# Optimization experiments

Measured on AMD Instinct MI355X. Metric: run time of the kernel, lower is better.

The kernel has to match this reference:

```python
import jax, jax.numpy as jnp
import numpy as np

TOP_K = 2  # config.top_k


def setup_inputs() -> dict:
    key = jax.random.key(0)
    k0, k1, k2, k3, k4 = jax.random.split(key, 5)
    B, S, D, F, E = 1, 2048, 512, 1024, 8
    scale = 0.02
    hidden_states = jax.random.normal(k0, (B, S, D), dtype=jnp.float32)
    router_w = jax.random.normal(k1, (D, E), dtype=jnp.float32) * scale
    w1 = jax.random.normal(k2, (E, D, F), dtype=jnp.float32) * scale  # gate proj
    w2 = jax.random.normal(k3, (E, F, D), dtype=jnp.float32) * scale  # down proj
    w3 = jax.random.normal(k4, (E, D, F), dtype=jnp.float32) * scale  # up proj
    return {"hidden_states": hidden_states, "router_w": router_w,
            "w1": w1, "w2": w2, "w3": w3}


def reference(hidden_states, router_w, w1, w2, w3):
    B, S, D = hidden_states.shape
    E = router_w.shape[1]
    x = hidden_states.reshape(-1, D)                      # [T, D]
    T = x.shape[0]

    # router: softmax in float32, top-k, renormalize (matches torch source)
    router_logits = x @ router_w                          # [T, E]
    probs = jax.nn.softmax(router_logits.astype(jnp.float32), axis=-1)
    routing_weights, selected_experts = jax.lax.top_k(probs, TOP_K)  # [T, K]
    routing_weights = routing_weights / routing_weights.sum(axis=-1, keepdims=True)
    routing_weights = routing_weights.astype(x.dtype)

    # combine weights: scatter top-k weights into dense [T, E] (one-hot combine)
    combine = jnp.zeros((T, E), dtype=x.dtype).at[
        jnp.arange(T)[:, None], selected_experts].add(routing_weights)

    # dense-all-experts evaluation, math-identical to gather-GEMM-scatter:
    # unselected experts get combine weight 0 and contribute nothing.
    gate = jax.nn.silu(jnp.einsum('td,edf->tef', x, w1))  # [T, E, F]
    up = jnp.einsum('td,edf->tef', x, w3)                 # [T, E, F]
    h = gate * up * combine[:, :, None]                   # weight before down-proj
    out = jnp.einsum('tef,efd->td', h, w2)                # [T, D]
    return out.reshape(B, S, D)
```

## Files before the change

kernel.cpp:

```cpp
#include <hip/hip_runtime.h>
#include <hip/hip_bf16.h>


typedef __attribute__((ext_vector_type(4))) float f32x4;
typedef __attribute__((ext_vector_type(8))) __bf16 bf16x8;

#define T_TOK 2048
#define DMODEL 512
#define FFN 1024
#define NE 8
#define MAXMB 40
#define PCAP (MAXMB * 128)

__device__ __forceinline__ void gload_lds16(const void* g, void* l) {
  __builtin_amdgcn_global_load_lds(
      (const __attribute__((address_space(1))) void*)g,
      (__attribute__((address_space(3))) void*)l, 16, 0, 0);
}

#define PIPE_BAR_8()                                        \
  asm volatile("s_waitcnt vmcnt(8)" ::: "memory");          \
  __builtin_amdgcn_s_barrier();                             \
  __builtin_amdgcn_sched_barrier(0)
#define PIPE_BAR_6()                                        \
  asm volatile("s_waitcnt vmcnt(6)" ::: "memory");          \
  __builtin_amdgcn_s_barrier();                             \
  __builtin_amdgcn_sched_barrier(0)
#define PIPE_BAR_0()                                        \
  asm volatile("s_waitcnt vmcnt(0)" ::: "memory");          \
  __builtin_amdgcn_s_barrier();                             \
  __builtin_amdgcn_sched_barrier(0)
#define POST_BAR()                                          \
  __builtin_amdgcn_s_barrier();                             \
  __builtin_amdgcn_sched_barrier(0)

__global__ __launch_bounds__(256) void prep_kernel(
    const float* __restrict__ x, const float* __restrict__ rw,
    const float* __restrict__ w1, const float* __restrict__ w2,
    const float* __restrict__ w3, __bf16* __restrict__ xb,
    __bf16* __restrict__ w1t, __bf16* __restrict__ w2t,
    __bf16* __restrict__ w3t, int* __restrict__ tope, float* __restrict__ topw,
    int* __restrict__ pair_t, float* __restrict__ pair_w,
    int* __restrict__ sched_e) {
  __shared__ __bf16 tile[64][65];
  const int bx = blockIdx.x;
  const int tid = threadIdx.x;

  if (bx < 3072) {
    const float* src;
    __bf16* dst;
    int R, C, idx;
    if (bx < 1024)      { src = w1; dst = w1t; R = 512;  C = 1024; idx = bx; }
    else if (bx < 2048) { src = w3; dst = w3t; R = 512;  C = 1024; idx = bx - 1024; }
    else                { src = w2; dst = w2t; R = 1024; C = 512;  idx = bx - 2048; }
    const int ntx = C >> 6, nty = R >> 6;
    const int cx = idx % ntx;
    const int gry = idx / ntx;
    const int e = gry / nty;
    const int r0 = (gry % nty) * 64;
    const int c0 = cx * 64;
    src += (size_t)e * R * C;
    dst += (size_t)e * R * C;
#pragma unroll
    for (int q = 0; q < 4; ++q) {
      const int r = (tid >> 4) + q * 16;
      const int c = (tid & 15) * 4;
      const f32x4 v = *(const f32x4*)&src[(size_t)(r0 + r) * C + c0 + c];
      tile[r][c] = (__bf16)v[0];
      tile[r][c + 1] = (__bf16)v[1];
      tile[r][c + 2] = (__bf16)v[2];
      tile[r][c + 3] = (__bf16)v[3];
    }
    __syncthreads();
#pragma unroll
    for (int p = 0; p < 2; ++p) {
      const int cc = (tid >> 3) + p * 32;
      const int rr = (tid & 7) * 8;
      union { bf16x8 v; __bf16 s[8]; } u;
#pragma unroll
      for (int i = 0; i < 8; ++i) u.s[i] = tile[rr + i][cc];
      *(bf16x8*)&dst[(size_t)(c0 + cc) * R + r0 + rr] = u.v;
    }
  } else if (bx < 3584) {
    const int t = (bx - 3072) * 4 + (tid >> 6);
    const int lane = tid & 63;
    const float* xr = x + (size_t)t * DMODEL + lane * 8;
    const f32x4 a = *(const f32x4*)xr;
    const f32x4 b = *(const f32x4*)(xr + 4);
    bf16x8 v;
    v[0] = (__bf16)a[0]; v[1] = (__bf16)a[1]; v[2] = (__bf16)a[2]; v[3] = (__bf16)a[3];
    v[4] = (__bf16)b[0]; v[5] = (__bf16)b[1]; v[6] = (__bf16)b[2]; v[7] = (__bf16)b[3];
    *(bf16x8*)&xb[(size_t)t * DMODEL + lane * 8] = v;

    float xv[8] = {a[0], a[1], a[2], a[3], b[0], b[1], b[2], b[3]};
    float part[NE];
#pragma unroll
    for (int e = 0; e < NE; ++e) part[e] = 0.f;
#pragma unroll
    for (int i = 0; i < 8; ++i) {
      const int d = lane * 8 + i;
      const f32x4 r0 = *(const f32x4*)&rw[(size_t)d * NE];
      const f32x4 r1 = *(const f32x4*)&rw[(size_t)d * NE + 4];
      part[0] += xv[i] * r0[0]; part[1] += xv[i] * r0[1];
      part[2] += xv[i] * r0[2]; part[3] += xv[i] * r0[3];
      part[4] += xv[i] * r1[0]; part[5] += xv[i] * r1[1];
      part[6] += xv[i] * r1[2]; part[7] += xv[i] * r1[3];
    }
#pragma unroll
    for (int off = 32; off > 0; off >>= 1) {
#pragma unroll
      for (int e = 0; e < NE; ++e) part[e] += __shfl_xor(part[e], off);
    }
    if (lane == 0) {
      int ia = 0;
#pragma unroll
      for (int e = 1; e < NE; ++e)
        if (part[e] > part[ia]) ia = e;
      int ib = (ia == 0) ? 1 : 0;
#pragma unroll
      for (int e = 0; e < NE; ++e)
        if (e != ia && e != ib && part[e] > part[ib]) ib = e;
      const float wa = 1.f / (1.f + __expf(part[ib] - part[ia]));
      tope[t * 2] = ia;
      tope[t * 2 + 1] = ib;
      topw[t * 2] = wa;
      topw[t * 2 + 1] = 1.f - wa;
    }
  } else {
    const int i = (bx - 3584) * 256 + tid;
    for (int j = i; j < PCAP; j += 2048) { pair_t[j] = 0; pair_w[j] = 0.f; }
    if (i < MAXMB) sched_e[i] = -1;
  }
}

__global__ __launch_bounds__(256) void build_kernel(
    const int* __restrict__ tope, const float* __restrict__ topw,
    int* __restrict__ pair_t, float* __restrict__ pair_w,
    int* __restrict__ pairidx, int* __restrict__ sched_e) {
  __shared__ int cnt[NE], base[NE], ofs[NE];
  const int tid = threadIdx.x;
  if (tid < NE) { cnt[tid] = 0; ofs[tid] = 0; }
  __syncthreads();
  for (int t = tid; t < T_TOK; t += 256) {
    atomicAdd(&cnt[tope[t * 2]], 1);
    atomicAdd(&cnt[tope[t * 2 + 1]], 1);
  }
  __syncthreads();
  if (tid == 0) {
    int mb = 0;
    for (int e = 0; e < NE; ++e) {
      base[e] = mb * 128;
      const int nmb = (cnt[e] + 127) >> 7;
      for (int i = 0; i < nmb; ++i) sched_e[mb + i] = e;
      mb += nmb;
    }
  }
  __syncthreads();
  for (int t = tid; t < T_TOK; t += 256) {
#pragma unroll
    for (int s = 0; s < 2; ++s) {
      const int e = tope[t * 2 + s];
      const int pos = base[e] + atomicAdd(&ofs[e], 1);
      pair_t[pos] = t;
      pair_w[pos] = topw[t * 2 + s];
      pairidx[t * 2 + s] = pos;
    }
  }
}

__global__ __launch_bounds__(256) void gemm1_kernel(
    const __bf16* __restrict__ xb, const __bf16* __restrict__ w1t,
    const __bf16* __restrict__ w3t, const int* __restrict__ pair_t,
    const float* __restrict__ pair_w, const int* __restrict__ sched_e,
    __bf16* __restrict__ hbuf) {
  __shared__ alignas(16) __bf16 As[2][128 * 64];
  __shared__ alignas(16) __bf16 B1s[2][64 * 64];
  __shared__ alignas(16) __bf16 B3s[2][64 * 64];
  __shared__ float comb[128];
  const int tid = threadIdx.x;
  const int id = blockIdx.x;
  const int mb = (id & 7) + ((id >> 7) << 3);
  const int f0 = ((id >> 3) & 15) * 64;
  const int e = sched_e[mb];
  if (e < 0) return;
  const int m0 = mb * 128;
  const int lane = tid & 63;
  const int wv = tid >> 6;
  const int wr = wv >> 1, wc = wv & 1;
  const int l15 = lane & 15, lhi = lane >> 4;
  const int sw = (l15 & 7) << 4;

  if (tid < 128) comb[tid] = pair_w[m0 + tid];

  size_t aoff[4];
  int lbA[4];
#pragma unroll
  for (int it = 0; it < 4; ++it) {
    const int chunk = it * 256 + tid;
    const int r = chunk >> 3;
    const int c8 = ((chunk & 7) ^ (r & 7)) * 8;
    aoff[it] = (size_t)pair_t[m0 + r] * DMODEL + c8;
    lbA[it] = (it * 256 + (tid & ~63)) * 16;
  }
  size_t boff[2];
  int lbB[2];
#pragma unroll
  for (int it = 0; it < 2; ++it) {
    const int chunk = it * 256 + tid;
    const int r = chunk >> 3;
    const int c8 = ((chunk & 7) ^ (r & 7)) * 8;
    boff[it] = (size_t)(e * FFN + f0 + r) * DMODEL + c8;
    lbB[it] = (it * 256 + (tid & ~63)) * 16;
  }

  const f32x4 fz = {0.f, 0.f, 0.f, 0.f};
  f32x4 acc1[4][2], acc3[4][2];
#pragma unroll
  for (int m = 0; m < 4; ++m)
#pragma unroll
    for (int n = 0; n < 2; ++n) { acc1[m][n] = fz; acc3[m][n] = fz; }

#define G1_STAGE(BUF, K0)                                                     \
  do {                                                                        \
    _Pragma("unroll") for (int it = 0; it < 4; ++it)                          \
        gload_lds16(xb + aoff[it] + (K0), (char*)As[BUF] + lbA[it]);          \
    _Pragma("unroll") for (int it = 0; it < 2; ++it) {                        \
      gload_lds16(w1t + boff[it] + (K0), (char*)B1s[BUF] + lbB[it]);          \
      gload_lds16(w3t + boff[it] + (K0), (char*)B3s[BUF] + lbB[it]);          \
    }                                                                         \
  } while (0)

#define G1_COMPUTE(BUF)                                                       \
  do {                                                                        \
    __builtin_amdgcn_s_setprio(1);                                            \
    _Pragma("unroll") for (int kk = 0; kk < 2; ++kk) {                        \
      const int ko = (kk * 64 + lhi * 16) ^ sw;                               \
      bf16x8 af[4], b1f[2], b3f[2];                                           \
      _Pragma("unroll") for (int m = 0; m < 4; ++m)                           \
          af[m] = *(const bf16x8*)((const char*)As[BUF] +                     \
                                   (wr * 64 + m * 16 + l15) * 128 + ko);      \
      _Pragma("unroll") for (int n = 0; n < 2; ++n) {                         \
        const int ro = (wc * 32 + n * 16 + l15) * 128 + ko;                   \
        b1f[n] = *(const bf16x8*)((const char*)B1s[BUF] + ro);                \
        b3f[n] = *(const bf16x8*)((const char*)B3s[BUF] + ro);                \
      }                                                                       \
      _Pragma("unroll") for (int m = 0; m < 4; ++m)                           \
          _Pragma("unroll") for (int n = 0; n < 2; ++n) {                     \
        acc1[m][n] = __builtin_amdgcn_mfma_f32_16x16x32_bf16(af[m], b1f[n],   \
                                                             acc1[m][n], 0, 0, 0); \
        acc3[m][n] = __builtin_amdgcn_mfma_f32_16x16x32_bf16(af[m], b3f[n],   \
                                                             acc3[m][n], 0, 0, 0); \
      }                                                                       \
    }                                                                         \
    __builtin_amdgcn_s_setprio(0);                                            \
  } while (0)

  G1_STAGE(0, 0);
#pragma unroll
  for (int t = 0; t < 7; ++t) {
    G1_STAGE((t + 1) & 1, (t + 1) * 64);
    PIPE_BAR_8();
    G1_COMPUTE(t & 1);
    POST_BAR();
  }
  PIPE_BAR_0();
  G1_COMPUTE(1);

  __syncthreads();
  {
    __bf16* eps = (__bf16*)As;
    constexpr int EW = 72;
#pragma unroll
    for (int m = 0; m < 4; ++m)
#pragma unroll
      for (int n = 0; n < 2; ++n)
#pragma unroll
        for (int r = 0; r < 4; ++r) {
          const int row = wr * 64 + m * 16 + lhi * 4 + r;
          const int col = wc * 32 + n * 16 + l15;
          const float g = acc1[m][n][r];
          const float u = acc3[m][n][r];
          eps[row * EW + col] = (__bf16)((g / (1.f + __expf(-g))) * u * comb[row]);
        }
    __syncthreads();
#pragma unroll
    for (int p = 0; p < 4; ++p) {
      const int i = p * 256 + tid;
      const int row = i >> 3, c8 = (i & 7) * 8;
      *(bf16x8*)&hbuf[(size_t)(m0 + row) * FFN + f0 + c8] =
          *(const bf16x8*)&eps[row * EW + c8];
    }
  }
#undef G1_STAGE
#undef G1_COMPUTE
}

__global__ __launch_bounds__(256) void gemm2_kernel(
    const __bf16* __restrict__ hbuf, const __bf16* __restrict__ w2t,
    const int* __restrict__ sched_e, __bf16* __restrict__ outp) {
  __shared__ alignas(16) __bf16 As[2][128 * 64];
  __shared__ alignas(16) __bf16 Bs[2][64 * 64];
  const int tid = threadIdx.x;
  const int id = blockIdx.x;
  const int gk = (id & 7) + ((id >> 6) << 3);
  const int n0 = ((id >> 3) & 7) * 64;
  const int mb = gk >> 1;
  const int kz = gk & 1;
  const int e = sched_e[mb];
  if (e < 0) return;
  const int m0 = mb * 128;
  const int fbase = kz * (FFN / 2);
  const int lane = tid & 63;
  const int wv = tid >> 6;
  const int wr = wv >> 1, wc = wv & 1;
  const int l15 = lane & 15, lhi = lane >> 4;
  const int sw = (l15 & 7) << 4;

  size_t aoff[4];
  int lbA[4];
#pragma unroll
  for (int it = 0; it < 4; ++it) {
    const int chunk = it * 256 + tid;
    const int r = chunk >> 3;
    const int c8 = ((chunk & 7) ^ (r & 7)) * 8;
    aoff[it] = (size_t)(m0 + r) * FFN + fbase + c8;
    lbA[it] = (it * 256 + (tid & ~63)) * 16;
  }
  size_t boff[2];
  int lbB[2];
#pragma unroll
  for (int it = 0; it < 2; ++it) {
    const int chunk = it * 256 + tid;
    const int r = chunk >> 3;
    const int c8 = ((chunk & 7) ^ (r & 7)) * 8;
    boff[it] = ((size_t)e * DMODEL + n0 + r) * FFN + fbase + c8;
    lbB[it] = (it * 256 + (tid & ~63)) * 16;
  }

  const f32x4 fz = {0.f, 0.f, 0.f, 0.f};
  f32x4 acc[4][2];
#pragma unroll
  for (int m = 0; m < 4; ++m) { acc[m][0] = fz; acc[m][1] = fz; }

#define G2_STAGE(BUF, K0)                                                     \
  do {                                                                        \
    _Pragma("unroll") for (int it = 0; it < 4; ++it)                          \
        gload_lds16(hbuf + aoff[it] + (K0), (char*)As[BUF] + lbA[it]);        \
    _Pragma("unroll") for (int it = 0; it < 2; ++it)                          \
        gload_lds16(w2t + boff[it] + (K0), (char*)Bs[BUF] + lbB[it]);         \
  } while (0)

#define G2_COMPUTE(BUF)                                                       \
  do {                                                                        \
    __builtin_amdgcn_s_setprio(1);                                            \
    _Pragma("unroll") for (int kk = 0; kk < 2; ++kk) {                        \
      const int ko = (kk * 64 + lhi * 16) ^ sw;                               \
      bf16x8 af[4], bfr[2];                                                   \
      _Pragma("unroll") for (int m = 0; m < 4; ++m)                           \
          af[m] = *(const bf16x8*)((const char*)As[BUF] +                     \
                                   (wr * 64 + m * 16 + l15) * 128 + ko);      \
      _Pragma("unroll") for (int n = 0; n < 2; ++n)                           \
          bfr[n] = *(const bf16x8*)((const char*)Bs[BUF] +                    \
                                    (wc * 32 + n * 16 + l15) * 128 + ko);     \
      _Pragma("unroll") for (int m = 0; m < 4; ++m)                           \
          _Pragma("unroll") for (int n = 0; n < 2; ++n)                       \
              acc[m][n] = __builtin_amdgcn_mfma_f32_16x16x32_bf16(            \
                  af[m], bfr[n], acc[m][n], 0, 0, 0);                         \
    }                                                                         \
    __builtin_amdgcn_s_setprio(0);                                            \
  } while (0)

  G2_STAGE(0, 0);
#pragma unroll
  for (int t = 0; t < 7; ++t) {
    G2_STAGE((t + 1) & 1, (t + 1) * 64);
    PIPE_BAR_6();
    G2_COMPUTE(t & 1);
    POST_BAR();
  }
  PIPE_BAR_0();
  G2_COMPUTE(1);

  __syncthreads();
  {
    __bf16* eps = (__bf16*)As;
    constexpr int EW = 72;
#pragma unroll
    for (int m = 0; m < 4; ++m)
#pragma unroll
      for (int n = 0; n < 2; ++n)
#pragma unroll
        for (int r = 0; r < 4; ++r) {
          const int row = wr * 64 + m * 16 + lhi * 4 + r;
          const int col = wc * 32 + n * 16 + l15;
          eps[row * EW + col] = (__bf16)acc[m][n][r];
        }
    __syncthreads();
#pragma unroll
    for (int p = 0; p < 4; ++p) {
      const int i = p * 256 + tid;
      const int row = i >> 3, c8 = (i & 7) * 8;
      *(bf16x8*)&outp[((size_t)kz * PCAP + m0 + row) * DMODEL + n0 + c8] =
          *(const bf16x8*)&eps[row * EW + c8];
    }
  }
#undef G2_STAGE
#undef G2_COMPUTE
}

__global__ __launch_bounds__(256) void gather_kernel(
    const __bf16* __restrict__ outp, const int* __restrict__ pairidx,
    float* __restrict__ out) {
  const int i = blockIdx.x * 256 + threadIdx.x;
  const int t = i >> 6;
  const int c = (i & 63) * 8;
  const int p0 = pairidx[t * 2];
  const int p1 = pairidx[t * 2 + 1];
  const size_t KZ = (size_t)PCAP * DMODEL;
  const bf16x8 a0 = *(const bf16x8*)&outp[(size_t)p0 * DMODEL + c];
  const bf16x8 a1 = *(const bf16x8*)&outp[(size_t)p1 * DMODEL + c];
  const bf16x8 b0 = *(const bf16x8*)&outp[KZ + (size_t)p0 * DMODEL + c];
  const bf16x8 b1 = *(const bf16x8*)&outp[KZ + (size_t)p1 * DMODEL + c];
  f32x4 lo, hi;
#pragma unroll
  for (int j = 0; j < 4; ++j)
    lo[j] = (float)a0[j] + (float)a1[j] + (float)b0[j] + (float)b1[j];
#pragma unroll
  for (int j = 0; j < 4; ++j)
    hi[j] = (float)a0[j + 4] + (float)a1[j + 4] + (float)b0[j + 4] + (float)b1[j + 4];
  float* op = out + (size_t)t * DMODEL + c;
  *(f32x4*)op = lo;
  *(f32x4*)(op + 4) = hi;
}

extern "C" void kernel_launch(void* const* d_in, const int* in_sizes, int n_in,
                              void* d_out, int out_size, void* d_ws, size_t ws_size,
                              hipStream_t stream) {
  const float* x = (const float*)d_in[0];
  const float* rw = (const float*)d_in[1];
  const float* w1 = (const float*)d_in[2];
  const float* w2 = (const float*)d_in[3];
  const float* w3 = (const float*)d_in[4];
  float* out = (float*)d_out;
  char* ws = (char*)d_ws;

  int* tope = (int*)(ws + 0);
  float* topw = (float*)(ws + 16384);
  int* pair_t = (int*)(ws + 32768);
  float* pair_w = (float*)(ws + 53248);
  int* pairidx = (int*)(ws + 73728);
  int* sched_e = (int*)(ws + 90112);
  __bf16* xb = (__bf16*)(ws + 98304);
  __bf16* w1t = (__bf16*)(ws + 2195456);
  __bf16* w3t = (__bf16*)(ws + 10584064);
  __bf16* w2t = (__bf16*)(ws + 18972672);
  __bf16* hbuf = (__bf16*)(ws + 27361280);
  __bf16* outp = (__bf16*)(ws + 37847040);

  hipLaunchKernelGGL(prep_kernel, dim3(3592), dim3(256), 0, stream,
                     x, rw, w1, w2, w3, xb, w1t, w2t, w3t, tope, topw,
                     pair_t, pair_w, sched_e);
  hipLaunchKernelGGL(build_kernel, dim3(1), dim3(256), 0, stream,
                     tope, topw, pair_t, pair_w, pairidx, sched_e);
  hipLaunchKernelGGL(gemm1_kernel, dim3(640), dim3(256), 0, stream,
                     xb, w1t, w3t, pair_t, pair_w, sched_e, hbuf);
  hipLaunchKernelGGL(gemm2_kernel, dim3(640), dim3(256), 0, stream,
                     hbuf, w2t, sched_e, outp);
  hipLaunchKernelGGL(gather_kernel, dim3(512), dim3(256), 0, stream,
                     outp, pairidx, out);
}
```

Measured before the change: 72.90 us.

## Interleave expert blocks, wave-aggregate routing atomics, triple-buffer gemm2 pipeline

The weight-conversion blocks and the GEMM grids now interleave experts in the low bits of the block index, so concurrently running blocks span different experts. Each expert gets a per-expert tile count and offset (meta) in place of a per-microblock schedule. The build kernel moves to 512 threads and uses wave ballots to combine LDS atomics for counting and slot assignment. gemm2 switches from two to three LDS buffers with a deeper vmcnt wait, which uses more shared memory and may lower occupancy. The new grid caps each expert at 8 tiles (MAXLOC), so skewed routing that gives one expert more than 1024 tokens would drop rows.

```diff
diff --git a/kernel.cpp b/kernel.cpp
--- a/kernel.cpp
+++ b/kernel.cpp
@@ -11,6 +11,7 @@
 #define NE 8
 #define MAXMB 40
 #define PCAP (MAXMB * 128)
+#define MAXLOC 8
 
 __device__ __forceinline__ void gload_lds16(const void* g, void* l) {
   __builtin_amdgcn_global_load_lds(
@@ -18,6 +19,10 @@
       (__attribute__((address_space(3))) void*)l, 16, 0, 0);
 }
 
+#define PIPE_BAR_12()                                       \
+  asm volatile("s_waitcnt vmcnt(12)" ::: "memory");         \
+  __builtin_amdgcn_s_barrier();                             \
+  __builtin_amdgcn_sched_barrier(0)
 #define PIPE_BAR_8()                                        \
   asm volatile("s_waitcnt vmcnt(8)" ::: "memory");          \
   __builtin_amdgcn_s_barrier();                             \
@@ -40,24 +45,25 @@
     const float* __restrict__ w3, __bf16* __restrict__ xb,
     __bf16* __restrict__ w1t, __bf16* __restrict__ w2t,
     __bf16* __restrict__ w3t, int* __restrict__ tope, float* __restrict__ topw,
-    int* __restrict__ pair_t, float* __restrict__ pair_w,
-    int* __restrict__ sched_e) {
+    int* __restrict__ pair_t, float* __restrict__ pair_w) {
   __shared__ __bf16 tile[64][65];
   const int bx = blockIdx.x;
   const int tid = threadIdx.x;
 
   if (bx < 3072) {
+    const int e = bx & 7;
+    const int rest = bx >> 3;
+    const int tsel = rest >> 7;
+    const int tidx = rest & 127;
     const float* src;
     __bf16* dst;
-    int R, C, idx;
-    if (bx < 1024)      { src = w1; dst = w1t; R = 512;  C = 1024; idx = bx; }
-    else if (bx < 2048) { src = w3; dst = w3t; R = 512;  C = 1024; idx = bx - 1024; }
-    else                { src = w2; dst = w2t; R = 1024; C = 512;  idx = bx - 2048; }
-    const int ntx = C >> 6, nty = R >> 6;
-    const int cx = idx % ntx;
-    const int gry = idx / ntx;
-    const int e = gry / nty;
-    const int r0 = (gry % nty) * 64;
+    int R, C;
+    if (tsel == 0)      { src = w1; dst = w1t; R = 512;  C = 1024; }
+    else if (tsel == 1) { src = w3; dst = w3t; R = 512;  C = 1024; }
+    else                { src = w2; dst = w2t; R = 1024; C = 512;  }
+    const int ntx = C >> 6;
+    const int cx = tidx % ntx;
+    const int r0 = (tidx / ntx) * 64;
     const int c0 = cx * 64;
     src += (size_t)e * R * C;
     dst += (size_t)e * R * C;
@@ -129,49 +135,66 @@
   } else {
     const int i = (bx - 3584) * 256 + tid;
     for (int j = i; j < PCAP; j += 2048) { pair_t[j] = 0; pair_w[j] = 0.f; }
-    if (i < MAXMB) sched_e[i] = -1;
-  }
-}
-
-__global__ __launch_bounds__(256) void build_kernel(
+  }
+}
+
+__global__ __launch_bounds__(512) void build_kernel(
     const int* __restrict__ tope, const float* __restrict__ topw,
     int* __restrict__ pair_t, float* __restrict__ pair_w,
-    int* __restrict__ pairidx, int* __restrict__ sched_e) {
+    int* __restrict__ pairidx, int* __restrict__ meta) {
   __shared__ int cnt[NE], base[NE], ofs[NE];
   const int tid = threadIdx.x;
+  const int lane = tid & 63;
   if (tid < NE) { cnt[tid] = 0; ofs[tid] = 0; }
   __syncthreads();
-  for (int t = tid; t < T_TOK; t += 256) {
-    atomicAdd(&cnt[tope[t * 2]], 1);
-    atomicAdd(&cnt[tope[t * 2 + 1]], 1);
+  for (int i = tid; i < T_TOK * 2; i += 512) {
+    const int e = tope[i];
+#pragma unroll
+    for (int ex = 0; ex < NE; ++ex) {
+      const unsigned long long m = __ballot(e == ex);
+      if (m != 0ull && lane == (__ffsll((long long)m) - 1))
+        atomicAdd(&cnt[ex], __popcll(m));
+    }
   }
   __syncthreads();
   if (tid == 0) {
     int mb = 0;
+#pragma unroll
     for (int e = 0; e < NE; ++e) {
+      const int nmb = (cnt[e] + 127) >> 7;
+      meta[e] = nmb;
+      meta[NE + e] = mb;
       base[e] = mb * 128;
-      const int nmb = (cnt[e] + 127) >> 7;
-      for (int i = 0; i < nmb; ++i) sched_e[mb + i] = e;
       mb += nmb;
     }
   }
   __syncthreads();
-  for (int t = tid; t < T_TOK; t += 256) {
-#pragma unroll
-    for (int s = 0; s < 2; ++s) {
-      const int e = tope[t * 2 + s];
-      const int pos = base[e] + atomicAdd(&ofs[e], 1);
-      pair_t[pos] = t;
-      pair_w[pos] = topw[t * 2 + s];
-      pairidx[t * 2 + s] = pos;
-    }
+  for (int i = tid; i < T_TOK * 2; i += 512) {
+    const int e = tope[i];
+    int pos = 0;
+#pragma unroll
+    for (int ex = 0; ex < NE; ++ex) {
+      const unsigned long long m = __ballot(e == ex);
+      if (e == ex) {
+        const int leader = __ffsll((long long)m) - 1;
+        const int nm = __popcll(m);
+        const int pre = __popcll(m & ((1ull << lane) - 1ull));
+        int start = 0;
+        if (lane == leader) start = atomicAdd(&ofs[ex], nm);
+        start = __shfl(start, leader);
+        pos = base[ex] + start + pre;
+      }
+    }
+    pair_t[pos] = i >> 1;
+    pair_w[pos] = topw[i];
+    pairidx[i] = pos;
   }
 }
 
 __global__ __launch_bounds__(256) void gemm1_kernel(
     const __bf16* __restrict__ xb, const __bf16* __restrict__ w1t,
     const __bf16* __restrict__ w3t, const int* __restrict__ pair_t,
-    const float* __restrict__ pair_w, const int* __restrict__ sched_e,
+    const float* __restrict__ pair_w, const int* __restrict__ meta,
     __bf16* __restrict__ hbuf) {
   __shared__ alignas(16) __bf16 As[2][128 * 64];
   __shared__ alignas(16) __bf16 B1s[2][64 * 64];
@@ -179,11 +202,11 @@
   __shared__ float comb[128];
   const int tid = threadIdx.x;
   const int id = blockIdx.x;
-  const int mb = (id & 7) + ((id >> 7) << 3);
+  const int e = id & 7;
   const int f0 = ((id >> 3) & 15) * 64;
-  const int e = sched_e[mb];
-  if (e < 0) return;
-  const int m0 = mb * 128;
+  const int local = id >> 7;
+  if (local >= meta[e]) return;
+  const int m0 = (meta[NE + e] + local) * 128;
   const int lane = tid & 63;
   const int wv = tid >> 6;
   const int wr = wv >> 1, wc = wv & 1;
@@ -297,18 +320,18 @@
 
 __global__ __launch_bounds__(256) void gemm2_kernel(
     const __bf16* __restrict__ hbuf, const __bf16* __restrict__ w2t,
-    const int* __restrict__ sched_e, __bf16* __restrict__ outp) {
-  __shared__ alignas(16) __bf16 As[2][128 * 64];
-  __shared__ alignas(16) __bf16 Bs[2][64 * 64];
+    const int* __restrict__ meta, __bf16* __restrict__ outp) {
+  __shared__ alignas(16) __bf16 As[3][128 * 64];
+  __shared__ alignas(16) __bf16 Bs[3][64 * 64];
   const int tid = threadIdx.x;
   const int id = blockIdx.x;
-  const int gk = (id & 7) + ((id >> 6) << 3);
-  const int n0 = ((id >> 3) & 7) * 64;
-  const int mb = gk >> 1;
-  const int kz = gk & 1;
-  const int e = sched_e[mb];
-  if (e < 0) return;
-  const int m0 = mb * 128;
+  const int e = id & 7;
+  const int j = id >> 3;
+  const int n0 = (j & 7) * 64;
+  const int kz = (j >> 3) & 1;
+  const int local = j >> 4;
+  if (local >= meta[e]) return;
+  const int m0 = (meta[NE + e] + local) * 128;
   const int fbase = kz * (FFN / 2);
   const int lane = tid & 63;
   const int wv = tid >> 6;
@@ -371,13 +394,17 @@
   } while (0)
 
   G2_STAGE(0, 0);
-#pragma unroll
-  for (int t = 0; t < 7; ++t) {
-    G2_STAGE((t + 1) & 1, (t + 1) * 64);
-    PIPE_BAR_6();
-    G2_COMPUTE(t & 1);
+  G2_STAGE(1, 64);
+#pragma unroll
+  for (int t = 0; t < 6; ++t) {
+    G2_STAGE((t + 2) % 3, (t + 2) * 64);
+    PIPE_BAR_12();
+    G2_COMPUTE(t % 3);
     POST_BAR();
   }
+  PIPE_BAR_6();
+  G2_COMPUTE(0);
+  POST_BAR();
   PIPE_BAR_0();
   G2_COMPUTE(1);
 
@@ -449,7 +476,7 @@
   int* pair_t = (int*)(ws + 32768);
   float* pair_w = (float*)(ws + 53248);
   int* pairidx = (int*)(ws + 73728);
-  int* sched_e = (int*)(ws + 90112);
+  int* meta = (int*)(ws + 90112);
   __bf16* xb = (__bf16*)(ws + 98304);
   __bf16* w1t = (__bf16*)(ws + 2195456);
   __bf16* w3t = (__bf16*)(ws + 10584064);
@@ -459,13 +486,13 @@
 
   hipLaunchKernelGGL(prep_kernel, dim3(3592), dim3(256), 0, stream,
                      x, rw, w1, w2, w3, xb, w1t, w2t, w3t, tope, topw,
-                     pair_t, pair_w, sched_e);
-  hipLaunchKernelGGL(build_kernel, dim3(1), dim3(256), 0, stream,
-                     tope, topw, pair_t, pair_w, pairidx, sched_e);
-  hipLaunchKernelGGL(gemm1_kernel, dim3(640), dim3(256), 0, stream,
-                     xb, w1t, w3t, pair_t, pair_w, sched_e, hbuf);
-  hipLaunchKernelGGL(gemm2_kernel, dim3(640), dim3(256), 0, stream,
-                     hbuf, w2t, sched_e, outp);
+                     pair_t, pair_w);
+  hipLaunchKernelGGL(build_kernel, dim3(1), dim3(512), 0, stream,
+                     tope, topw, pair_t, pair_w, pairidx, meta);
+  hipLaunchKernelGGL(gemm1_kernel, dim3(8 * 16 * MAXLOC), dim3(256), 0, stream,
+                     xb, w1t, w3t, pair_t, pair_w, meta, hbuf);
+  hipLaunchKernelGGL(gemm2_kernel, dim3(8 * 8 * 2 * MAXLOC), dim3(256), 0, stream,
+                     hbuf, w2t, meta, outp);
   hipLaunchKernelGGL(gather_kernel, dim3(512), dim3(256), 0, stream,
                      outp, pairidx, out);
 }
```

Measured after the change: 85.46 us. 1.17x slower.
